# Optimization experiments

Measured on AMD Instinct MI355X. Metric: run time of the kernel, lower is better.

The kernel has to match this reference:

```python
import jax, jax.numpy as jnp
import numpy as np
from jax import lax

B, N = 16, 8192          # batch, points per cloud
G, K = 512, 32           # num_groups, group_size
TOKEN_DIM = 384
BN_EPS = 1e-5


def setup_inputs() -> dict:
    key = jax.random.key(0)
    ks = jax.random.split(key, 8)
    w = lambda i, shape: jax.random.normal(ks[i], shape, jnp.float32) * 0.05
    return {
        "points": jax.random.normal(ks[0], (B, N, 3), jnp.float32),
        # first_conv: Conv1d(3,128,1,bias=False) -> BN(128) -> ReLU -> Conv1d(128,256,1)
        "w1": w(1, (128, 3)),
        "bn1_gamma": jnp.ones((128,), jnp.float32),
        "bn1_beta": jnp.zeros((128,), jnp.float32),
        "bn1_mean": jnp.zeros((128,), jnp.float32),
        "bn1_var": jnp.ones((128,), jnp.float32),
        "w2": w(2, (256, 128)),
        "b2": jnp.zeros((256,), jnp.float32),
        # second_conv: Conv1d(512,512,1,bias=False) -> BN(512) -> ReLU -> Conv1d(512,384,1)
        "w3": w(3, (512, 512)),
        "bn2_gamma": jnp.ones((512,), jnp.float32),
        "bn2_beta": jnp.zeros((512,), jnp.float32),
        "bn2_mean": jnp.zeros((512,), jnp.float32),
        "bn2_var": jnp.ones((512,), jnp.float32),
        "w4": w(4, (TOKEN_DIM, 512)),
        "b4": jnp.zeros((TOKEN_DIM,), jnp.float32),
    }


def _fps(xyz, num_samples):
    """Farthest point sampling. xyz: [B,N,3] -> idx [B,num_samples] (start = point 0)."""
    b, n, _ = xyz.shape
    start = jnp.zeros((b,), jnp.int32)
    init_min = jnp.full((b, n), 1e10, xyz.dtype)

    def body(carry, _):
        min_d2, last = carry
        last_pt = jnp.take_along_axis(xyz, last[:, None, None], axis=1)  # [B,1,3]
        d2 = jnp.sum((xyz - last_pt) ** 2, axis=-1)                      # [B,N]
        min_d2 = jnp.minimum(min_d2, d2)
        nxt = jnp.argmax(min_d2, axis=-1).astype(jnp.int32)
        return (min_d2, nxt), last

    _, idx = lax.scan(body, (init_min, start), None, length=num_samples)
    return idx.T  # [B,num_samples]


def _bn(x, gamma, beta, mean, var):
    # inference batchnorm over last (channel) axis
    return (x - mean) * lax.rsqrt(var + BN_EPS) * gamma + beta


def reference(points, w1, bn1_gamma, bn1_beta, bn1_mean, bn1_var, w2, b2,
              w3, bn2_gamma, bn2_beta, bn2_mean, bn2_var, w4, b4):
    xyz = points[:, :, :3]
    fidx = _fps(xyz, G)                                       # [B,G]
    centers = jnp.take_along_axis(xyz, fidx[:, :, None], 1)   # [B,G,3]

    # brute-force KNN via squared distances [B,G,N]
    pn = jnp.sum(xyz * xyz, -1)                               # [B,N]
    cn = jnp.sum(centers * centers, -1)                       # [B,G]
    d2 = cn[:, :, None] + pn[:, None, :] - 2.0 * jnp.einsum('bgc,bnc->bgn', centers, xyz)
    _, idx = lax.top_k(-d2, K)                                # [B,G,K] nearest indices

    groups = jax.vmap(lambda p, i: p[i])(points, idx)          # [B,G,K,3]
    groups = groups - centers[:, :, None, :]                   # center-relative coords

    x = groups.reshape(B * G, K, 3)                            # [M,K,3]
    # first_conv
    f = jnp.einsum('mkc,dc->mkd', x, w1)                       # [M,K,128]
    f = jax.nn.relu(_bn(f, bn1_gamma, bn1_beta, bn1_mean, bn1_var))
    f = jnp.einsum('mkd,ed->mke', f, w2) + b2                  # [M,K,256]
    g = jnp.max(f, axis=1, keepdims=True)                      # [M,1,256]
    f = jnp.concatenate([jnp.broadcast_to(g, f.shape), f], -1) # [M,K,512]
    # second_conv
    f = jnp.einsum('mke,fe->mkf', f, w3)                       # [M,K,512]
    f = jax.nn.relu(_bn(f, bn2_gamma, bn2_beta, bn2_mean, bn2_var))
    f = jnp.einsum('mkf,of->mko', f, w4) + b4                  # [M,K,384]
    tokens = jnp.max(f, axis=1).reshape(B, G, TOKEN_DIM)
    return tokens, centers
```

## Files before the change

### kernel.cpp

```cpp
#include <hip/hip_runtime.h>
#include <stdint.h>

#define PB 16
#define PN 8192
#define PG 512
#define PK 32
#define PTOK 384
#define PM (PB*PG)
#define PMK (PM*PK)
#define NWORK 240
#define NTASK (PM/4)
static constexpr float BN_EPS_C = 1e-5f;

typedef short bh8  __attribute__((ext_vector_type(8)));
typedef float f32x4 __attribute__((ext_vector_type(4)));

__device__ __forceinline__ short f2bf(float f){
  unsigned u = __float_as_uint(f);
  unsigned r = u + 0x7fffu + ((u>>16)&1u);
  return (short)(r>>16);
}
__device__ __forceinline__ float bf2f(short s){
  return __uint_as_float(((unsigned)(unsigned short)s)<<16);
}
__device__ __forceinline__ void gload16(const void* g, void* l){
  __builtin_amdgcn_global_load_lds((const __attribute__((address_space(1))) unsigned int*)g,
                                   (__attribute__((address_space(3))) unsigned int*)l,
                                   16, 0, 0);
}

__global__ __launch_bounds__(1024, 4) void mega2_kernel(
    const float* __restrict__ points, float* __restrict__ centers,
    int* __restrict__ prog, int* __restrict__ qhead,
    float* __restrict__ grp){
#pragma clang fp contract(off)
  __shared__ __align__(16) char SMEM[150528];
  const int t = threadIdx.x;
  const int lane = t & 63;

  if (blockIdx.x < PB){
    const int b = blockIdx.x;
    const float* P = points + (size_t)b*PN*3;
    float4* Lc = (float4*)SMEM;
    unsigned short* sidx = (unsigned short*)(SMEM + 131072);
    int* shist = (int*)(SMEM + 147456);
    int* spart = (int*)(SMEM + 149504);
    unsigned long long* swa = (unsigned long long*)(SMEM + 149760);
    if (t < 512) shist[t] = 0;
    if (t < 3)   swa[t] = 0ull;
    __syncthreads();
    int mycell[8];
#pragma unroll
    for (int i=0;i<8;i++){
      int j = i*1024 + t;
      float x=P[j*3+0], y=P[j*3+1], z=P[j*3+2];
      Lc[j] = make_float4(x,y,z,0.f);
      int qx=(int)fminf(fmaxf((x+4.f)*1.0f,0.f),7.f);
      int qy=(int)fminf(fmaxf((y+4.f)*1.0f,0.f),7.f);
      int qz=(int)fminf(fmaxf((z+4.f)*1.0f,0.f),7.f);
      int mc = (qx&1)|((qx&2)<<2)|((qx&4)<<4)
             | ((qy&1)<<1)|((qy&2)<<3)|((qy&4)<<5)
             | ((qz&1)<<2)|((qz&2)<<4)|((qz&4)<<6);
      mycell[i]=mc;
      atomicAdd(&shist[mc],1);
    }
    __syncthreads();
    if (t < 64){
      int acc=0;
#pragma unroll
      for (int k=0;k<8;k++){ int h=shist[t*8+k]; shist[t*8+k]=acc; acc+=h; }
      spart[t]=acc;
    }
    __syncthreads();
    if (t==0){ int acc=0; for (int k=0;k<64;k++){ int h=spart[k]; spart[k]=acc; acc+=h; } }
    __syncthreads();
    if (t < 64){
      int off=spart[t];
#pragma unroll
      for (int k=0;k<8;k++) shist[t*8+k] += off;
    }
    __syncthreads();
#pragma unroll
    for (int i=0;i<8;i++){
      int j = i*1024 + t;
      int r = atomicAdd(&shist[mycell[i]],1);
      sidx[r] = (unsigned short)j;
    }
    __syncthreads();
    float px[8],py[8],pz[8],md[8]; int lowc[8];
    float tlx=1e30f,tly=1e30f,tlz=1e30f,thx=-1e30f,thy=-1e30f,thz=-1e30f;
#pragma unroll
    for (int i=0;i<8;i++){
      int oj = sidx[t*8+i];
      float4 p4 = Lc[oj];
      float x=p4.x, y=p4.y, z=p4.z;
      px[i]=x; py[i]=y; pz[i]=z; md[i]=1e10f; lowc[i]=PN-1-oj;
      tlx=fminf(tlx,x); thx=fmaxf(thx,x);
      tly=fminf(tly,y); thy=fmaxf(thy,y);
      tlz=fminf(tlz,z); thz=fmaxf(thz,z);
    }
#pragma unroll
    for (int off=32; off; off>>=1){
      tlx=fminf(tlx,__shfl_xor(tlx,off)); thx=fmaxf(thx,__shfl_xor(thx,off));
      tly=fminf(tly,__shfl_xor(tly,off)); thy=fmaxf(thy,__shfl_xor(thy,off));
      tlz=fminf(tlz,__shfl_xor(tlz,off)); thz=fmaxf(thz,__shfl_xor(thz,off));
    }
    unsigned long long wkey = ((unsigned long long)0x7F800000u)<<32;
    float cx=P[0], cy=P[1], cz=P[2];
    if (t==0){ float* c = centers + (size_t)b*PG*3; c[0]=cx; c[1]=cy; c[2]=cz; }
    __syncthreads();
    for (int g=1; g<PG; g++){
      const int sl = g%3, ns = (g+1)%3;
      float ddx=fmaxf(fmaxf(tlx-cx, cx-thx),0.f);
      float ddy=fmaxf(fmaxf(tly-cy, cy-thy),0.f);
      float ddz=fmaxf(fmaxf(tlz-cz, cz-thz),0.f);
      float dmin2=((ddx*ddx+ddy*ddy)+ddz*ddz)*0.999999f;
      if (!(dmin2 >= __uint_as_float((unsigned)(wkey>>32)))){
        unsigned long long bk = 0ull;
#pragma unroll
        for (int i=0;i<8;i++){
          float dx=px[i]-cx, dy=py[i]-cy, dz=pz[i]-cz;
          float d2 = (dx*dx + dy*dy) + dz*dz;
          md[i] = fminf(md[i], d2);
          unsigned long long ki = ((unsigned long long)__float_as_uint(md[i])<<32)
                                | (unsigned)lowc[i];
          if (ki > bk) bk = ki;
        }
#pragma unroll
        for (int mask=32; mask; mask>>=1){
          unsigned long long o = __shfl_xor(bk, mask);
          if (o > bk) bk = o;
        }
        wkey = bk;
      }
      if (lane==0) atomicMax(&swa[sl], wkey);
      if (t==0) swa[ns] = 0ull;
      __syncthreads();
      unsigned long long w = swa[sl];
      int j = PN-1 - (int)(w & 0xFFFFFFFFu);
      float4 c4 = Lc[j];
      cx = c4.x; cy = c4.y; cz = c4.z;
      if (t==0){
        float* cc = centers + ((size_t)b*PG + g)*3;
        cc[0]=cx; cc[1]=cy; cc[2]=cz;
        if ((g & 3) == 3)
          __hip_atomic_store(prog + b, g + 1, __ATOMIC_RELEASE, __HIP_MEMORY_SCOPE_AGENT);
      }
    }
  }

  unsigned* s_hist = (unsigned*)SMEM;
  unsigned long long* s_surv = (unsigned long long*)(SMEM + 4096);
  int*   s_sct   = (int*)(SMEM + 6144);
  int*   s_bparm = (int*)(SMEM + 6160);
  int*   s_flag  = (int*)(SMEM + 6192);
  float* ks_c    = (float*)(SMEM + 6208);
  int*   s_task  = (int*)(SMEM + 6256);
  unsigned long long* ks_k = (unsigned long long*)(SMEM + 149504);
  int*   ks_idx  = (int*)(SMEM + 149760);

  for(;;){
    if (t == 0){
      int id = atomicAdd(qhead, 1);
      s_task[0] = id;
      if (id < NTASK){
        int bb = id & (PB-1), qq = id >> 4;
        int need = qq*4 + 4;
        while (__hip_atomic_load(prog + bb, __ATOMIC_ACQUIRE, __HIP_MEMORY_SCOPE_AGENT) < need)
          __builtin_amdgcn_s_sleep(10);
      }
    }
    __syncthreads();
    const int id = s_task[0];
    if (id >= NTASK) break;
    const int b = id & (PB-1), q = id >> 4;
    const int m0 = b*PG + q*4;
    const float* P = points + (size_t)b*PN*3;
    const int sub = t >> 8, tt = t & 255;
    const int swv = tt >> 6;

    s_hist[t] = 0;
    if (t < 4)  s_sct[t] = 0;
    if (t == 0) s_flag[0] = 0;
    if (tt == 0){
      const float* cp = centers + (size_t)(m0 + sub)*3;
      ks_c[sub*3+0] = __hip_atomic_load(cp+0, __ATOMIC_ACQUIRE, __HIP_MEMORY_SCOPE_AGENT);
      ks_c[sub*3+1] = __hip_atomic_load(cp+1, __ATOMIC_ACQUIRE, __HIP_MEMORY_SCOPE_AGENT);
      ks_c[sub*3+2] = __hip_atomic_load(cp+2, __ATOMIC_ACQUIRE, __HIP_MEMORY_SCOPE_AGENT);
    }
    __syncthreads();

    const float cx=ks_c[sub*3+0], cy=ks_c[sub*3+1], cz=ks_c[sub*3+2];
    const float cn = (cx*cx + cy*cy) + cz*cz;
    unsigned key[PK];
#pragma unroll
    for (int i=0;i<PK;i++){
      int j = i*256 + tt;
      float x=P[j*3+0], y=P[j*3+1], z=P[j*3+2];
      float pn = (x*x + y*y) + z*z;
      float e  = (cx*x + cy*y) + cz*z;
      float d2 = (cn + pn) - 2.0f*e;
      unsigned u = __float_as_uint(d2);
      u ^= (u & 0x80000000u) ? 0xFFFFFFFFu : 0x80000000u;
      key[i] = u;
      atomicAdd(&s_hist[sub*256 + (u>>24)], 1u);
    }
    __syncthreads();

    int B = 0, nless = 0;
    if (swv == 0){
      unsigned v0 = s_hist[sub*256 + lane*4 + 0];
      unsigned v1 = s_hist[sub*256 + lane*4 + 1];
      unsigned v2 = s_hist[sub*256 + lane*4 + 2];
      unsigned v3 = s_hist[sub*256 + lane*4 + 3];
      unsigned tot = ((v0 + v1) + v2) + v3;
      unsigned inc = tot;
      for (int off=1; off<64; off<<=1){
        unsigned n = __shfl_up(inc, off);
        if (lane >= off) inc += n;
      }
      unsigned excl = inc - tot;
      unsigned c0 = excl + v0, c1 = c0 + v1, c2 = c1 + v2, c3 = c2 + v3;
      int cand = 1<<30;
      if (c3 >= 32u){
        cand = lane*4 + 3;
        if (c2 >= 32u) cand = lane*4 + 2;
        if (c1 >= 32u) cand = lane*4 + 1;
        if (c0 >= 32u) cand = lane*4 + 0;
      }
      int Bc = cand;
      for (int m=32; m; m>>=1){ int o = __shfl_xor(Bc, m); if (o < Bc) Bc = o; }
      int src = Bc >> 2, kk = Bc & 3;
      unsigned cc01 = (c0 & 0xFFFFu) | (c1 << 16);
      unsigned cc23 = (c2 & 0xFFFFu) | (c3 << 16);
      unsigned vv01 = (v0 & 0xFFFFu) | (v1 << 16);
      unsigned vv23 = (v2 & 0xFFFFu) | (v3 << 16);
      unsigned a01 = __shfl(cc01, src), a23 = __shfl(cc23, src);
      unsigned w01 = __shfl(vv01, src), w23 = __shfl(vv23, src);
      unsigned Sincl = (kk==0) ? (a01 & 0xFFFFu) : (kk==1) ? (a01 >> 16)
                     : (kk==2) ? (a23 & 0xFFFFu) : (a23 >> 16);
      unsigned vB    = (kk==0) ? (w01 & 0xFFFFu) : (kk==1) ? (w01 >> 16)
                     : (kk==2) ? (w23 & 0xFFFFu) : (w23 >> 16);
      B = Bc; nless = (int)(Sincl - vB);
      if (tt == 0) s_bparm[sub*2+0] = B;
    }
    __syncthreads();
    B = s_bparm[sub*2+0];
    s_hist[t] = 0;
    __syncthreads();

#pragma unroll
    for (int i=0;i<PK;i++){
      unsigned u = key[i];
      if ((int)(u>>24) == B) atomicAdd(&s_hist[sub*256 + ((u>>16)&255u)], 1u);
    }
    __syncthreads();

    if (swv == 0){
      unsigned v0 = s_hist[sub*256 + lane*4 + 0];
      unsigned v1 = s_hist[sub*256 + lane*4 + 1];
      unsigned v2 = s_hist[sub*256 + lane*4 + 2];
      unsigned v3 = s_hist[sub*256 + lane*4 + 3];
      unsigned tot = ((v0 + v1) + v2) + v3;
      unsigned inc = tot;
      for (int off=1; off<64; off<<=1){
        unsigned n = __shfl_up(inc, off);
        if (lane >= off) inc += n;
      }
      unsigned excl = inc - tot;
      unsigned c0 = excl + v0, c1 = c0 + v1, c2 = c1 + v2, c3 = c2 + v3;
      unsigned thr = 32u - (unsigned)nless;
      int cand = 1<<30;
      if (c3 >= thr){
        cand = lane*4 + 3;
        if (c2 >= thr) cand = lane*4 + 2;
        if (c1 >= thr) cand = lane*4 + 1;
        if (c0 >= thr) cand = lane*4 + 0;
      }
      int Bc = cand;
      for (int m=32; m; m>>=1){ int o = __shfl_xor(Bc, m); if (o < Bc) Bc = o; }
      int src = Bc >> 2, kk = Bc & 3;
      unsigned cc01 = (c0 & 0xFFFFu) | (c1 << 16);
      unsigned cc23 = (c2 & 0xFFFFu) | (c3 << 16);
      unsigned a01 = __shfl(cc01, src), a23 = __shfl(cc23, src);
      unsigned Sincl = (kk==0) ? (a01 & 0xFFFFu) : (kk==1) ? (a01 >> 16)
                     : (kk==2) ? (a23 & 0xFFFFu) : (a23 >> 16);
      int S2 = nless + (int)Sincl;
      if (tt == 0){
        s_bparm[sub*2+1] = Bc;
        if (S2 > 64) s_flag[0] = 1;
      }
    }
    if (swv == 1) s_surv[sub*64 + lane] = ~0ull;
    __syncthreads();
    const int B2 = s_bparm[sub*2+1];
    const int doFB = s_flag[0];

    if (!doFB){
#pragma unroll
      for (int i=0;i<PK;i++){
        unsigned u = key[i];
        int hb = (int)(u >> 24), b2v = (int)((u >> 16) & 255u);
        if (hb < B || (hb == B && b2v <= B2)){
          int ix = atomicAdd(&s_sct[sub], 1);
          if (ix < 64)
            s_surv[sub*64 + ix] = ((unsigned long long)u << 32) | (unsigned)(i*256 + tt);
        }
      }
    }
    __syncthreads();
    if (!doFB){
      if (swv == 0){
        unsigned long long v = s_surv[sub*64 + lane];
        for (int k=2; k<=64; k<<=1)
          for (int j2=k>>1; j2>=1; j2>>=1){
            unsigned long long o = __shfl_xor(v, j2);
            bool keepMin = (((lane & j2) == 0) == ((lane & k) == 0));
            unsigned long long mn = (v < o) ? v : o;
            unsigned long long mx = (v < o) ? o : v;
            v = keepMin ? mn : mx;
          }
        if (lane < PK){
          int j = (int)(v & 0xFFFFFFFFull);
#pragma unroll
          for (int c=0;c<3;c++)
            grp[((size_t)(m0+sub)*PK + lane)*3 + c] = P[j*3+c] - ks_c[sub*3+c];
        }
      }
    } else {
      unsigned lmin = key[0]; int li = 0;
#pragma unroll
      for (int i=1;i<PK;i++) if (key[i] < lmin){ lmin = key[i]; li = i; }
      unsigned long long lkey = ((unsigned long long)lmin << 32)
                              | (unsigned)(li*256 + tt);
      const int widx = tt >> 6;
      for (int it=0; it<PK; it++){
        unsigned long long v = lkey;
#pragma unroll
        for (int off=32; off; off>>=1){
          unsigned long long o = __shfl_down(v, off);
          if (o < v) v = o;
        }
        if (lane==0) ks_k[sub*8 + (it&1)*4 + widx] = v;
        __syncthreads();
        unsigned long long w = ks_k[sub*8 + (it&1)*4 + 0];
#pragma unroll
        for (int qq=1;qq<4;qq++){
          unsigned long long o = ks_k[sub*8 + (it&1)*4 + qq];
          if (o < w) w = o;
        }
        int wj = (int)(w & 0xFFFFFFFFull);
        if (tt==0) ks_idx[sub*32 + it] = wj;
        if ((wj & 255) == tt){
          int slot = wj >> 8;
#pragma unroll
          for (int i=0;i<PK;i++) if (i == slot) key[i] = 0xFFFFFFFFu;
          lmin = key[0]; li = 0;
#pragma unroll
          for (int i=1;i<PK;i++) if (key[i] < lmin){ lmin = key[i]; li = i; }
          lkey = ((unsigned long long)lmin << 32) | (unsigned)(li*256 + tt);
        }
      }
      __syncthreads();
      if (tt < PK*3){
        int k = tt/3, c = tt - k*3;
        int j = ks_idx[sub*32 + k];
        grp[((size_t)(m0 + sub)*PK + k)*3 + c] = P[j*3+c] - ks_c[sub*3+c];
      }
    }
  }
}

__global__ __launch_bounds__(512, 2) void mlp_kernel(const float* __restrict__ grp,
                                                     const float* __restrict__ w1,
                                                     const float* __restrict__ sc1,
                                                     const float* __restrict__ sh1,
                                                     const short* __restrict__ w2b,
                                                     const float* __restrict__ b2,
                                                     const short* __restrict__ w3ab,
                                                     const short* __restrict__ w3bb,
                                                     const float* __restrict__ sc2,
                                                     const float* __restrict__ sh2,
                                                     const short* __restrict__ w4b,
                                                     const float* __restrict__ b4,
                                                     float* __restrict__ tokens){
  __shared__ __align__(16) short s_f1f3[16384];
  __shared__ __align__(16) short s_f2[32768];
  __shared__ __align__(16) short s_g[1024];
  __shared__ __align__(16) short s_bst[24576];
  const int t = threadIdx.x;
  const int lane = t & 63, wid = t >> 6;
  const int mh = wid >> 1, nq = wid & 1;
  const int B0 = blockIdx.x * 128;
  const int G0 = blockIdx.x * 4;
  const int srow = lane >> 2;
  const int scol = (lane & 3) * 8;
  const int frow = lane & 15;
  const int fk   = (lane >> 4) * 8;
  const int rb   = (lane >> 4) * 4;
  const int cb   = lane & 15;

  {
    int r = t & 127, dg = t >> 7;
    float x0 = grp[(size_t)(B0+r)*3 + 0];
    float x1 = grp[(size_t)(B0+r)*3 + 1];
    float x2 = grp[(size_t)(B0+r)*3 + 2];
#pragma unroll
    for (int dd=0; dd<32; dd++){
      int d = dg*32 + dd;
      float a = x0*w1[d*3+0] + x1*w1[d*3+1] + x2*w1[d*3+2];
      float y = a*sc1[d] + sh1[d];
      s_f1f3[dg*4096 + r*32 + dd] = f2bf(fmaxf(y, 0.f));
    }
  }
  __syncthreads();

  {
    f32x4 accB[2][8] = {};
    for (int k0=0; k0<128; k0+=64){
      for (int cc=wid; cc<32; cc+=8){
        int sub = cc & 1, rc = cc >> 1;
        int r = rc*16 + srow;
        gload16(w2b + (size_t)r*128 + k0 + sub*32 + scol, &s_bst[sub*8192 + rc*512]);
      }
      __syncthreads();
#pragma unroll
      for (int sub=0; sub<2; sub++){
        int kc = (k0 + sub*32) >> 5;
        bh8 af[2], bf[8];
#pragma unroll
        for (int i=0;i<2;i++)
          af[i] = *(const bh8*)&s_f1f3[kc*4096 + (mh*32 + i*16 + frow)*32 + fk];
#pragma unroll
        for (int j=0;j<8;j++)
          bf[j] = *(const bh8*)&s_bst[sub*8192 + (nq*128 + j*16 + frow)*32 + fk];
#pragma unroll
        for (int i=0;i<2;i++)
#pragma unroll
          for (int j=0;j<8;j++)
            accB[i][j] = __builtin_amdgcn_mfma_f32_16x16x32_bf16(af[i], bf[j], accB[i][j], 0,0,0);
      }
      __syncthreads();
    }
#pragma unroll
    for (int i=0;i<2;i++)
#pragma unroll
      for (int j=0;j<8;j++){
        int col = nq*128 + j*16 + cb;
#pragma unroll
        for (int r=0;r<4;r++){
          int row = mh*32 + i*16 + rb + r;
          s_f2[(col>>5)*4096 + row*32 + (col&31)] = f2bf(accB[i][j][r] + b2[col]);
        }
      }
  }
  __syncthreads();

  {
#pragma unroll
    for (int task=0; task<2; task++){
      int g = (t>>8) + task*2;
      int col = t & 255;
      int kc = col >> 5, c5 = col & 31;
      float mx = -3.4e38f;
#pragma unroll
      for (int kk=0; kk<PK; kk++)
        mx = fmaxf(mx, bf2f(s_f2[kc*4096 + (g*32 + kk)*32 + c5]));
      s_g[g*256 + col] = f2bf(mx);
    }
  }
  __syncthreads();

  f32x4 acc4[2][12] = {};
  for (int nc=0; nc<4; nc++){
    f32x4 acc3[2][4] = {};
    for (int k0=0; k0<512; k0+=64){
      const short* w3s = (k0 < 256) ? w3ab : w3bb;
      int kk0 = (k0 < 256) ? k0 : (k0 - 256);
      for (int cc=wid; cc<16; cc+=8){
        int sub = cc & 1, rc = cc >> 1;
        int r = nc*128 + rc*16 + srow;
        gload16(w3s + (size_t)r*256 + kk0 + sub*32 + scol, &s_bst[sub*4096 + rc*512]);
      }
      __syncthreads();
#pragma unroll
      for (int sub=0; sub<2; sub++){
        int k = k0 + sub*32;
        bh8 af[2], bf[4];
        if (k < 256){
#pragma unroll
          for (int i=0;i<2;i++)
            af[i] = *(const bh8*)&s_g[mh*256 + k + fk];
        } else {
          int kc = (k - 256) >> 5;
#pragma unroll
          for (int i=0;i<2;i++)
            af[i] = *(const bh8*)&s_f2[kc*4096 + (mh*32 + i*16 + frow)*32 + fk];
        }
#pragma unroll
        for (int j=0;j<4;j++)
          bf[j] = *(const bh8*)&s_bst[sub*4096 + (nq*64 + j*16 + frow)*32 + fk];
#pragma unroll
        for (int i=0;i<2;i++)
#pragma unroll
          for (int j=0;j<4;j++)
            acc3[i][j] = __builtin_amdgcn_mfma_f32_16x16x32_bf16(af[i], bf[j], acc3[i][j], 0,0,0);
      }
      __syncthreads();
    }
#pragma unroll
    for (int i=0;i<2;i++)
#pragma unroll
      for (int j=0;j<4;j++){
        int cl = nq*64 + j*16 + cb;
        int f  = nc*128 + cl;
        float s = sc2[f], h = sh2[f];
#pragma unroll
        for (int r=0;r<4;r++){
          int row = mh*32 + i*16 + rb + r;
          float v = acc3[i][j][r]*s + h;
          s_f1f3[(cl>>5)*4096 + row*32 + (cl&31)] = f2bf(fmaxf(v, 0.f));
        }
      }
    __syncthreads();
    for (int kk0=0; kk0<128; kk0+=64){
      for (int cc=wid; cc<48; cc+=8){
        int sub = cc & 1, rc = cc >> 1;
        int r = rc*16 + srow;
        gload16(w4b + (size_t)r*512 + nc*128 + kk0 + sub*32 + scol, &s_bst[sub*12288 + rc*512]);
      }
      __syncthreads();
#pragma unroll
      for (int sub=0; sub<2; sub++){
        int kc = (kk0 + sub*32) >> 5;
        bh8 af[2], bf[12];
#pragma unroll
        for (int i=0;i<2;i++)
          af[i] = *(const bh8*)&s_f1f3[kc*4096 + (mh*32 + i*16 + frow)*32 + fk];
#pragma unroll
        for (int j=0;j<12;j++)
          bf[j] = *(const bh8*)&s_bst[sub*12288 + (nq*192 + j*16 + frow)*32 + fk];
#pragma unroll
        for (int i=0;i<2;i++)
#pragma unroll
          for (int j=0;j<12;j++)
            acc4[i][j] = __builtin_amdgcn_mfma_f32_16x16x32_bf16(af[i], bf[j], acc4[i][j], 0,0,0);
      }
      __syncthreads();
    }
  }

#pragma unroll
  for (int j=0;j<12;j++){
    int col = nq*192 + j*16 + cb;
    float mx = -3.4e38f;
#pragma unroll
    for (int i=0;i<2;i++)
#pragma unroll
      for (int r=0;r<4;r++)
        mx = fmaxf(mx, acc4[i][j][r]);
    mx = fmaxf(mx, __shfl_xor(mx, 16));
    mx = fmaxf(mx, __shfl_xor(mx, 32));
    if (lane < 16)
      tokens[(size_t)(G0 + mh)*PTOK + col] = mx + b4[col];
  }
}

__global__ __launch_bounds__(256) void prep_kernel(const float* __restrict__ w2,
    const float* __restrict__ w3, const float* __restrict__ w4,
    const float* __restrict__ g1, const float* __restrict__ be1,
    const float* __restrict__ mu1, const float* __restrict__ va1,
    const float* __restrict__ g2, const float* __restrict__ be2,
    const float* __restrict__ mu2, const float* __restrict__ va2,
    short* __restrict__ w2b, short* __restrict__ w3ab, short* __restrict__ w3bb,
    short* __restrict__ w4b, float* __restrict__ sc1, float* __restrict__ sh1,
    float* __restrict__ sc2, float* __restrict__ sh2,
    int* __restrict__ prog, int* __restrict__ qhead){
  int i = blockIdx.x*256 + threadIdx.x;
  if (i < 256*128) w2b[i] = f2bf(w2[i]);
  if (i < 512*512){
    int f = i >> 9, e = i & 511;
    short v = f2bf(w3[i]);
    if (e < 256) w3ab[f*256 + e] = v; else w3bb[f*256 + (e-256)] = v;
  }
  if (i < 384*512) w4b[i] = f2bf(w4[i]);
  if (i < 128){ float s = g1[i]*rsqrtf(va1[i] + BN_EPS_C); sc1[i]=s; sh1[i]=be1[i]-mu1[i]*s; }
  if (i < 512){ float s = g2[i]*rsqrtf(va2[i] + BN_EPS_C); sc2[i]=s; sh2[i]=be2[i]-mu2[i]*s; }
  if (i < PB) prog[i] = 0;
  if (i == PB) qhead[0] = 0;
}

extern "C" void kernel_launch(void* const* d_in, const int* in_sizes, int n_in,
                              void* d_out, int out_size, void* d_ws, size_t ws_size,
                              hipStream_t stream){
  const float* points = (const float*)d_in[0];
  const float* w1  = (const float*)d_in[1];
  const float* g1  = (const float*)d_in[2];
  const float* be1 = (const float*)d_in[3];
  const float* mu1 = (const float*)d_in[4];
  const float* va1 = (const float*)d_in[5];
  const float* w2  = (const float*)d_in[6];
  const float* b2  = (const float*)d_in[7];
  const float* w3  = (const float*)d_in[8];
  const float* g2  = (const float*)d_in[9];
  const float* be2 = (const float*)d_in[10];
  const float* mu2 = (const float*)d_in[11];
  const float* va2 = (const float*)d_in[12];
  const float* w4  = (const float*)d_in[13];
  const float* b4  = (const float*)d_in[14];
  float* tokens  = (float*)d_out;
  float* centers = (float*)d_out + (size_t)PM*PTOK;

  char* ws = (char*)d_ws;
  float* grp  = (float*)(ws + 0);
  short* w2b  = (short*)(ws + 3145728ull);
  short* w3ab = (short*)(ws + 3211264ull);
  short* w3bb = (short*)(ws + 3473408ull);
  short* w4b  = (short*)(ws + 3735552ull);
  float* sc1  = (float*)(ws + 4128768ull);
  float* sh1  = (float*)(ws + 4129280ull);
  float* sc2  = (float*)(ws + 4129792ull);
  float* sh2  = (float*)(ws + 4131840ull);
  int*   prog = (int*)(ws + 4133888ull);
  int*   qhead= (int*)(ws + 4133952ull);

  prep_kernel<<<1024, 256, 0, stream>>>(w2, w3, w4, g1, be1, mu1, va1, g2, be2, mu2, va2,
                                        w2b, w3ab, w3bb, w4b, sc1, sh1, sc2, sh2,
                                        prog, qhead);
  mega2_kernel<<<PB + NWORK, 1024, 0, stream>>>(points, centers, prog, qhead, grp);
  mlp_kernel<<<PMK/128, 512, 0, stream>>>(grp, w1, sc1, sh1, w2b, b2,
                                          w3ab, w3bb, sc2, sh2, w4b, b4, tokens);
}
```

Baseline: 1.062 ms.

## Halve MLP block tile to 64 rows for higher occupancy

Each MLP block now handles 64 point rows (2 groups) instead of 128 (4 groups). Each wave covers 16 rows instead of 32, so LDS per block and accumulator registers are halved, and launch bounds request 4 blocks per CU. Max pooling now goes through a small shared reduction, since each group spans two wave rows. The cost is that every block reloads the full w2/w3/w4 weight tiles into LDS for half the rows, which doubles weight traffic and barrier count per unit of work.

Result: slower. 1.115 ms (+5.0%).

```diff
diff --git a/kernel.cpp b/kernel.cpp
--- a/kernel.cpp
+++ b/kernel.cpp
@@ -371,7 +371,7 @@
   }
 }
 
-__global__ __launch_bounds__(512, 2) void mlp_kernel(const float* __restrict__ grp,
+__global__ __launch_bounds__(512, 4) void mlp_kernel(const float* __restrict__ grp,
                                                      const float* __restrict__ w1,
                                                      const float* __restrict__ sc1,
                                                      const float* __restrict__ sh1,
@@ -384,15 +384,16 @@
                                                      const short* __restrict__ w4b,
                                                      const float* __restrict__ b4,
                                                      float* __restrict__ tokens){
-  __shared__ __align__(16) short s_f1f3[16384];
-  __shared__ __align__(16) short s_f2[32768];
-  __shared__ __align__(16) short s_g[1024];
-  __shared__ __align__(16) short s_bst[24576];
+  __shared__ __align__(16) short s_f1f3[8192];
+  __shared__ __align__(16) short s_f2[16384];
+  __shared__ __align__(16) short s_g[512];
+  __shared__ __align__(16) short s_bst[12288];
+  float* s_pool = (float*)s_bst;
   const int t = threadIdx.x;
   const int lane = t & 63, wid = t >> 6;
   const int mh = wid >> 1, nq = wid & 1;
-  const int B0 = blockIdx.x * 128;
-  const int G0 = blockIdx.x * 4;
+  const int B0 = blockIdx.x * 64;
+  const int G0 = blockIdx.x * 2;
   const int srow = lane >> 2;
   const int scol = (lane & 3) * 8;
   const int frow = lane & 15;
@@ -401,151 +402,118 @@
   const int cb   = lane & 15;
 
   {
-    int r = t & 127, dg = t >> 7;
+    int r = t & 63, dg = t >> 6;
     float x0 = grp[(size_t)(B0+r)*3 + 0];
     float x1 = grp[(size_t)(B0+r)*3 + 1];
     float x2 = grp[(size_t)(B0+r)*3 + 2];
 #pragma unroll
-    for (int dd=0; dd<32; dd++){
-      int d = dg*32 + dd;
+    for (int dd=0; dd<16; dd++){
+      int d = dg*16 + dd;
       float a = x0*w1[d*3+0] + x1*w1[d*3+1] + x2*w1[d*3+2];
       float y = a*sc1[d] + sh1[d];
-      s_f1f3[dg*4096 + r*32 + dd] = f2bf(fmaxf(y, 0.f));
+      s_f1f3[(d>>5)*2048 + r*32 + (d&31)] = f2bf(fmaxf(y, 0.f));
     }
   }
   __syncthreads();
 
   {
-    f32x4 accB[2][8] = {};
-    for (int k0=0; k0<128; k0+=64){
-      for (int cc=wid; cc<32; cc+=8){
-        int sub = cc & 1, rc = cc >> 1;
-        int r = rc*16 + srow;
-        gload16(w2b + (size_t)r*128 + k0 + sub*32 + scol, &s_bst[sub*8192 + rc*512]);
-      }
-      __syncthreads();
-#pragma unroll
-      for (int sub=0; sub<2; sub++){
-        int kc = (k0 + sub*32) >> 5;
-        bh8 af[2], bf[8];
-#pragma unroll
-        for (int i=0;i<2;i++)
-          af[i] = *(const bh8*)&s_f1f3[kc*4096 + (mh*32 + i*16 + frow)*32 + fk];
-#pragma unroll
-        for (int j=0;j<8;j++)
-          bf[j] = *(const bh8*)&s_bst[sub*8192 + (nq*128 + j*16 + frow)*32 + fk];
-#pragma unroll
-        for (int i=0;i<2;i++)
-#pragma unroll
-          for (int j=0;j<8;j++)
-            accB[i][j] = __builtin_amdgcn_mfma_f32_16x16x32_bf16(af[i], bf[j], accB[i][j], 0,0,0);
-      }
-      __syncthreads();
-    }
-#pragma unroll
-    for (int i=0;i<2;i++)
-#pragma unroll
-      for (int j=0;j<8;j++){
-        int col = nq*128 + j*16 + cb;
-#pragma unroll
-        for (int r=0;r<4;r++){
-          int row = mh*32 + i*16 + rb + r;
-          s_f2[(col>>5)*4096 + row*32 + (col&31)] = f2bf(accB[i][j][r] + b2[col]);
-        }
-      }
+    f32x4 accB[8] = {};
+    for (int k0=0; k0<128; k0+=32){
+      for (int cc=wid; cc<16; cc+=8)
+        gload16(w2b + (size_t)(cc*16+srow)*128 + k0 + scol, &s_bst[cc*512]);
+      __syncthreads();
+      int kc = k0 >> 5;
+      bh8 af = *(const bh8*)&s_f1f3[kc*2048 + (mh*16 + frow)*32 + fk];
+      bh8 bf[8];
+#pragma unroll
+      for (int j=0;j<8;j++)
+        bf[j] = *(const bh8*)&s_bst[(nq*128 + j*16 + frow)*32 + fk];
+#pragma unroll
+      for (int j=0;j<8;j++)
+        accB[j] = __builtin_amdgcn_mfma_f32_16x16x32_bf16(af, bf[j], accB[j], 0,0,0);
+      __syncthreads();
+    }
+#pragma unroll
+    for (int j=0;j<8;j++){
+      int col = nq*128 + j*16 + cb;
+#pragma unroll
+      for (int r=0;r<4;r++){
+        int row = mh*16 + rb + r;
+        s_f2[(col>>5)*2048 + row*32 + (col&31)] = f2bf(accB[j][r] + b2[col]);
+      }
+    }
   }
   __syncthreads();
 
   {
-#pragma unroll
-    for (int task=0; task<2; task++){
-      int g = (t>>8) + task*2;
-      int col = t & 255;
-      int kc = col >> 5, c5 = col & 31;
-      float mx = -3.4e38f;
-#pragma unroll
-      for (int kk=0; kk<PK; kk++)
-        mx = fmaxf(mx, bf2f(s_f2[kc*4096 + (g*32 + kk)*32 + c5]));
-      s_g[g*256 + col] = f2bf(mx);
-    }
+    int g = t >> 8, col = t & 255;
+    int kc = col >> 5, c5 = col & 31;
+    float mx = -3.4e38f;
+#pragma unroll
+    for (int kk=0; kk<PK; kk++)
+      mx = fmaxf(mx, bf2f(s_f2[kc*2048 + (g*32 + kk)*32 + c5]));
+    s_g[g*256 + col] = f2bf(mx);
   }
   __syncthreads();
 
-  f32x4 acc4[2][12] = {};
+  f32x4 acc4[12] = {};
   for (int nc=0; nc<4; nc++){
-    f32x4 acc3[2][4] = {};
+    f32x4 acc3[4] = {};
     for (int k0=0; k0<512; k0+=64){
       const short* w3s = (k0 < 256) ? w3ab : w3bb;
-      int kk0 = (k0 < 256) ? k0 : (k0 - 256);
+      int kb = (k0 < 256) ? k0 : (k0 - 256);
       for (int cc=wid; cc<16; cc+=8){
         int sub = cc & 1, rc = cc >> 1;
-        int r = nc*128 + rc*16 + srow;
-        gload16(w3s + (size_t)r*256 + kk0 + sub*32 + scol, &s_bst[sub*4096 + rc*512]);
+        gload16(w3s + (size_t)(nc*128 + rc*16 + srow)*256 + kb + sub*32 + scol,
+                &s_bst[sub*4096 + rc*512]);
       }
       __syncthreads();
 #pragma unroll
       for (int sub=0; sub<2; sub++){
         int k = k0 + sub*32;
-        bh8 af[2], bf[4];
+        bh8 af;
         if (k < 256){
-#pragma unroll
-          for (int i=0;i<2;i++)
-            af[i] = *(const bh8*)&s_g[mh*256 + k + fk];
+          af = *(const bh8*)&s_g[(mh>>1)*256 + k + fk];
         } else {
           int kc = (k - 256) >> 5;
-#pragma unroll
-          for (int i=0;i<2;i++)
-            af[i] = *(const bh8*)&s_f2[kc*4096 + (mh*32 + i*16 + frow)*32 + fk];
-        }
+          af = *(const bh8*)&s_f2[kc*2048 + (mh*16 + frow)*32 + fk];
+        }
+        bh8 bf[4];
 #pragma unroll
         for (int j=0;j<4;j++)
           bf[j] = *(const bh8*)&s_bst[sub*4096 + (nq*64 + j*16 + frow)*32 + fk];
 #pragma unroll
-        for (int i=0;i<2;i++)
-#pragma unroll
-          for (int j=0;j<4;j++)
-            acc3[i][j] = __builtin_amdgcn_mfma_f32_16x16x32_bf16(af[i], bf[j], acc3[i][j], 0,0,0);
-      }
-      __syncthreads();
-    }
-#pragma unroll
-    for (int i=0;i<2;i++)
-#pragma unroll
-      for (int j=0;j<4;j++){
-        int cl = nq*64 + j*16 + cb;
-        int f  = nc*128 + cl;
-        float s = sc2[f], h = sh2[f];
-#pragma unroll
-        for (int r=0;r<4;r++){
-          int row = mh*32 + i*16 + rb + r;
-          float v = acc3[i][j][r]*s + h;
-          s_f1f3[(cl>>5)*4096 + row*32 + (cl&31)] = f2bf(fmaxf(v, 0.f));
-        }
-      }
-    __syncthreads();
-    for (int kk0=0; kk0<128; kk0+=64){
-      for (int cc=wid; cc<48; cc+=8){
-        int sub = cc & 1, rc = cc >> 1;
-        int r = rc*16 + srow;
-        gload16(w4b + (size_t)r*512 + nc*128 + kk0 + sub*32 + scol, &s_bst[sub*12288 + rc*512]);
-      }
-      __syncthreads();
-#pragma unroll
-      for (int sub=0; sub<2; sub++){
-        int kc = (kk0 + sub*32) >> 5;
-        bh8 af[2], bf[12];
-#pragma unroll
-        for (int i=0;i<2;i++)
-          af[i] = *(const bh8*)&s_f1f3[kc*4096 + (mh*32 + i*16 + frow)*32 + fk];
-#pragma unroll
-        for (int j=0;j<12;j++)
-          bf[j] = *(const bh8*)&s_bst[sub*12288 + (nq*192 + j*16 + frow)*32 + fk];
-#pragma unroll
-        for (int i=0;i<2;i++)
-#pragma unroll
-          for (int j=0;j<12;j++)
-            acc4[i][j] = __builtin_amdgcn_mfma_f32_16x16x32_bf16(af[i], bf[j], acc4[i][j], 0,0,0);
-      }
+        for (int j=0;j<4;j++)
+          acc3[j] = __builtin_amdgcn_mfma_f32_16x16x32_bf16(af, bf[j], acc3[j], 0,0,0);
+      }
+      __syncthreads();
+    }
+#pragma unroll
+    for (int j=0;j<4;j++){
+      int cl = nq*64 + j*16 + cb;
+      int f  = nc*128 + cl;
+      float s = sc2[f], h = sh2[f];
+#pragma unroll
+      for (int r=0;r<4;r++){
+        int row = mh*16 + rb + r;
+        float v = acc3[j][r]*s + h;
+        s_f1f3[(cl>>5)*2048 + row*32 + (cl&31)] = f2bf(fmaxf(v, 0.f));
+      }
+    }
+    __syncthreads();
+    for (int kk0=0; kk0<128; kk0+=32){
+      for (int cc=wid; cc<24; cc+=8)
+        gload16(w4b + (size_t)(cc*16+srow)*512 + nc*128 + kk0 + scol, &s_bst[cc*512]);
+      __syncthreads();
+      int kc = kk0 >> 5;
+      bh8 af = *(const bh8*)&s_f1f3[kc*2048 + (mh*16 + frow)*32 + fk];
+      bh8 bf[12];
+#pragma unroll
+      for (int j=0;j<12;j++)
+        bf[j] = *(const bh8*)&s_bst[(nq*192 + j*16 + frow)*32 + fk];
+#pragma unroll
+      for (int j=0;j<12;j++)
+        acc4[j] = __builtin_amdgcn_mfma_f32_16x16x32_bf16(af, bf[j], acc4[j], 0,0,0);
       __syncthreads();
     }
   }
@@ -553,16 +521,16 @@
 #pragma unroll
   for (int j=0;j<12;j++){
     int col = nq*192 + j*16 + cb;
-    float mx = -3.4e38f;
-#pragma unroll
-    for (int i=0;i<2;i++)
-#pragma unroll
-      for (int r=0;r<4;r++)
-        mx = fmaxf(mx, acc4[i][j][r]);
+    float mx = fmaxf(fmaxf(acc4[j][0], acc4[j][1]), fmaxf(acc4[j][2], acc4[j][3]));
     mx = fmaxf(mx, __shfl_xor(mx, 16));
     mx = fmaxf(mx, __shfl_xor(mx, 32));
-    if (lane < 16)
-      tokens[(size_t)(G0 + mh)*PTOK + col] = mx + b4[col];
+    if (lane < 16) s_pool[mh*384 + col] = mx;
+  }
+  __syncthreads();
+  for (int p = t; p < 768; p += 512){
+    int g = p / 384, c = p - g*384;
+    float m = fmaxf(s_pool[(2*g)*384 + c], s_pool[(2*g+1)*384 + c]);
+    tokens[(size_t)(G0 + g)*PTOK + c] = m + b4[c];
   }
 }
 
@@ -628,6 +596,6 @@
                                         w2b, w3ab, w3bb, w4b, sc1, sh1, sc2, sh2,
                                         prog, qhead);
   mega2_kernel<<<PB + NWORK, 1024, 0, stream>>>(points, centers, prog, qhead, grp);
-  mlp_kernel<<<PMK/128, 512, 0, stream>>>(grp, w1, sc1, sh1, w2b, b2,
-                                          w3ab, w3bb, sc2, sh2, w4b, b4, tokens);
+  mlp_kernel<<<PMK/64, 512, 0, stream>>>(grp, w1, sc1, sh1, w2b, b2,
+                                         w3ab, w3bb, sc2, sh2, w4b, b4, tokens);
 }
```
